# Kernel optimization log

Hardware: AMD Instinct MI355X
Metric: run time of the kernel (lower is better)

The kernel has to match this reference:

```python
import jax, jax.numpy as jnp
import numpy as np

EPS = 1e-5  # BatchNorm1d default eps

def _conv1d(x, w, stride, pad):
    # x: [B, Cin, L], w: [Cout, Cin, K]
    return jax.lax.conv_general_dilated(
        x, w, window_strides=(stride,), padding=[(pad, pad)],
        dimension_numbers=('NCH', 'OIH', 'NCH'))

def _bn(x, g, b, m, v):
    # eval-mode BatchNorm1d with running stats; x: [B, C, L]
    scale = g / jnp.sqrt(v + EPS)
    return x * scale[None, :, None] + (b - m * scale)[None, :, None]

def _hardtanh(x):
    return jnp.clip(x, -1.0, 1.0)

def _maxpool2(x):
    B, C, L = x.shape
    return x.reshape(B, C, L // 2, 2).max(axis=-1)


def setup_inputs() -> dict:
    key = jax.random.key(0)
    ks = jax.random.split(key, 20)
    B, L = 256, 16384
    x = jax.random.normal(ks[0], (B, 1, L), dtype=jnp.float32)
    rms = jax.random.uniform(ks[1], (B, 1), dtype=jnp.float32)
    # conv weights (fan-in scaled)
    w1 = jax.random.normal(ks[2], (16, 1, 17), dtype=jnp.float32) * (1.0 / np.sqrt(1 * 17))
    w2 = jax.random.normal(ks[3], (32, 16, 9), dtype=jnp.float32) * (1.0 / np.sqrt(16 * 9))
    w3 = jax.random.normal(ks[4], (64, 32, 5), dtype=jnp.float32) * (1.0 / np.sqrt(32 * 5))
    # batchnorm params (eval mode: gamma, beta, running mean/var)
    def bn_params(k, C):
        k1, k2, k3, k4 = jax.random.split(k, 4)
        g = 1.0 + 0.1 * jax.random.normal(k1, (C,), dtype=jnp.float32)
        b = 0.1 * jax.random.normal(k2, (C,), dtype=jnp.float32)
        m = 0.1 * jax.random.normal(k3, (C,), dtype=jnp.float32)
        v = jax.random.uniform(k4, (C,), dtype=jnp.float32, minval=0.5, maxval=1.5)
        return g, b, m, v
    g1, b1, m1, v1 = bn_params(ks[5], 16)
    g2, b2, m2, v2 = bn_params(ks[6], 32)
    g3, b3, m3, v3 = bn_params(ks[7], 64)
    fc1_w = jax.random.normal(ks[8], (32, 65), dtype=jnp.float32) * (1.0 / np.sqrt(65))
    fc1_b = jnp.zeros((32,), dtype=jnp.float32)
    fc2_w = jax.random.normal(ks[9], (2, 32), dtype=jnp.float32) * (1.0 / np.sqrt(32))
    fc2_b = jnp.zeros((2,), dtype=jnp.float32)
    return dict(x=x, rms=rms, w1=w1, g1=g1, b1=b1, m1=m1, v1=v1,
                w2=w2, g2=g2, b2=b2, m2=m2, v2=v2,
                w3=w3, g3=g3, b3=b3, m3=m3, v3=v3,
                fc1_w=fc1_w, fc1_b=fc1_b, fc2_w=fc2_w, fc2_b=fc2_b)


def reference(x, rms, w1, g1, b1, m1, v1, w2, g2, b2, m2, v2,
              w3, g3, b3, m3, v3, fc1_w, fc1_b, fc2_w, fc2_b):
    # Stage 1: float conv
    h = _conv1d(x, w1, 2, 8)                 # [B,16,8192]
    h = _maxpool2(_hardtanh(_bn(h, g1, b1, m1, v1)))  # [B,16,4096]
    # Stage 2: binarized (sign) weight conv
    h = _conv1d(h, jnp.sign(w2), 2, 4)       # [B,32,2048]
    h = _maxpool2(_hardtanh(_bn(h, g2, b2, m2, v2)))  # [B,32,1024]
    # Stage 3: binarized weight conv
    h = _conv1d(h, jnp.sign(w3), 2, 2)       # [B,64,512]
    h = _maxpool2(_hardtanh(_bn(h, g3, b3, m3, v3)))  # [B,64,256]
    feat = h.mean(axis=-1)                   # AdaptiveAvgPool1d(1) -> [B,64]
    combined = jnp.concatenate([feat, rms], axis=1)   # [B,65]
    h = _hardtanh(combined @ fc1_w.T + fc1_b)
    return h @ fc2_w.T + fc2_b               # [B,2]
```

## Files before the change

### kernel.cpp

```cpp
#include <hip/hip_runtime.h>
#include <hip/hip_bf16.h>

#define EPS 1e-5f

typedef float f32x4 __attribute__((ext_vector_type(4)));
typedef short s16x8 __attribute__((ext_vector_type(8)));

union FragU { uint4 u; s16x8 s; };

__device__ __forceinline__ float ht(float x){ return __builtin_amdgcn_fmed3f(x, -1.f, 1.f); }
__device__ __forceinline__ float sgn(float v){ return (v>0.f)?1.f:((v<0.f)?-1.f:0.f); }
__device__ __forceinline__ unsigned short f2bf(float f){
    unsigned int u = __builtin_bit_cast(unsigned int, f);
    u += 0x7FFFu + ((u>>16)&1u);
    return (unsigned short)(u>>16);
}
__device__ __forceinline__ unsigned pkbf(float a, float b){
    __hip_bfloat162 h = __float22bfloat162_rn(float2{a, b});
    unsigned u;
    __builtin_memcpy(&u, &h, sizeof(u));
    return u;
}

__global__ __launch_bounds__(512) void prep(
    const float* __restrict__ w1, const float* __restrict__ w2, const float* __restrict__ w3,
    const float* g1,const float* b1,const float* m1,const float* v1,
    const float* g2,const float* b2,const float* m2,const float* v2,
    const float* g3,const float* b3,const float* m3,const float* v3,
    unsigned short* __restrict__ a1, unsigned short* __restrict__ a2,
    unsigned short* __restrict__ a3, float* __restrict__ bn){
  const int t = threadIdx.x, bid = blockIdx.x;
  if(bid == 0){
    if(t < 64){
      int q = t>>4, m = t&15;
      #pragma unroll
      for(int j=0;j<8;++j){ int k = 8*q+j;
        a1[t*8+j] = f2bf((k<17)? w1[m*17+k] : 0.f); }
    }
    if(t<16){ float s = g1[t]*rsqrtf(v1[t]+EPS); bn[t]    = s; bn[16+t]  = b1[t]-m1[t]*s; }
    if(t<32){ float s = g2[t]*rsqrtf(v2[t]+EPS); bn[32+t] = s; bn[64+t]  = b2[t]-m2[t]*s; }
    if(t<64){ float s = g3[t]*rsqrtf(v3[t]+EPS); bn[96+t] = s; bn[160+t] = b3[t]-m3[t]*s; }
  } else if(bid <= 2){
    int e = (bid-1)*512 + t;
    if(e < 640){
      int m = e&15, q = (e>>4)&3, hc = e>>6, c = hc%5, h = hc/5;
      int oc = m + 16*h, k = 2*c + (q>>1);
      #pragma unroll
      for(int j=0;j<8;++j){ int ic = 8*(q&1)+j;
        a2[e*8+j] = f2bf((k<9)? sgn(w2[(oc*16+ic)*9+k]) : 0.f); }
    }
  } else {
    int e = (bid-3)*512 + t;
    if(e < 1280){
      int m = e&15, q = (e>>4)&3, gc = e>>6, c = gc%5, g = gc/5;
      int oc = m + 16*g;
      #pragma unroll
      for(int j=0;j<8;++j){ int ic = 8*q+j;
        a3[e*8+j] = f2bf(sgn(w3[(oc*32+ic)*5+c])); }
    }
  }
}

__global__ __launch_bounds__(256, 4) void kfused(const float* __restrict__ x,
    const unsigned short* __restrict__ a1, const unsigned short* __restrict__ a2,
    const unsigned short* __restrict__ a3, const float* __restrict__ bn,
    float* __restrict__ partial){
  __shared__ __align__(16) unsigned short xs[1216];
  __shared__ __align__(16) unsigned short s1[296*26];
  __shared__ __align__(16) unsigned short s2[68*42];
  __shared__ float fws[4*32];
  const int b  = blockIdx.x >> 3;
  const int tp = blockIdx.x & 7;
  const int tid = threadIdx.x;
  const int m = tid & 15, q = (tid & 63) >> 4, w = tid >> 6;
  const int tw = w & 1, gw = w >> 1;
  const float* xrow = &x[b*16384];

  FragU af1; af1.u = *(const uint4*)&a1[(q*16+m)*8];
  const float sc1 = bn[m], sh1 = bn[16+m];

  for(int u = 0; u < 2; ++u){
    const int t  = 2*tp + u;
    const int Q0 = 16*t;

    const int x0 = 64*Q0 - 56;
    for(int i = tid; i < 304; i += 256){
      int g0 = x0 + 4*i;
      float4 v = make_float4(0.f,0.f,0.f,0.f);
      if(g0 >= 0 && g0 <= 16380) v = *(const float4*)&xrow[g0];
      uint2 pk;
      pk.x = pkbf(v.x, v.y);
      pk.y = pkbf(v.z, v.w);
      *(uint2*)&xs[4*i] = pk;
    }
    __syncthreads();

    const unsigned* X32 = (const unsigned*)xs;
    #pragma unroll 2
    for(int it = 0; it < 10; ++it){
      int tile = it*4 + w;
      if(tile < 37){
        int d = tile*16 + m + 4*q;
        FragU bf;
        bf.u.x = X32[d]; bf.u.y = X32[d+1]; bf.u.z = X32[d+2]; bf.u.w = X32[d+3];
        f32x4 acc = {0.f,0.f,0.f,0.f};
        acc = __builtin_amdgcn_mfma_f32_16x16x32_bf16(bf.s, af1.s, acc, 0,0,0);
        float v0 = ht(acc[0]*sc1 + sh1);
        float v1 = ht(acc[1]*sc1 + sh1);
        float v2 = ht(acc[2]*sc1 + sh1);
        float v3 = ht(acc[3]*sc1 + sh1);
        int ppl = tile*8 + 2*q;
        int gp  = 16*Q0 - 12 + ppl;
        float p0 = ((unsigned)gp     < 4096u) ? fmaxf(v0, v1) : 0.f;
        float p1 = ((unsigned)(gp+1) < 4096u) ? fmaxf(v2, v3) : 0.f;
        unsigned uu = pkbf(p0, p1);
        s1[ppl*26 + m]     = (unsigned short)uu;
        s1[(ppl+1)*26 + m] = (unsigned short)(uu >> 16);
      }
    }
    __syncthreads();

    FragU af2[2][5];
    #pragma unroll
    for(int h=0;h<2;++h)
      #pragma unroll
      for(int c=0;c<5;++c)
        af2[h][c].u = *(const uint4*)&a2[(((h*5+c)*4+q)*16+m)*8];
    float sc2[2], sh2[2];
    #pragma unroll
    for(int h=0;h<2;++h){
      sc2[h] = bn[32 + m + 16*h];
      sh2[h] = bn[64 + m + 16*h];
    }
    #pragma unroll
    for(int it = 0; it < 3; ++it){
      int tile = it*4 + w;
      if(tile < 9){
        int nl = tile*16 + m;
        f32x4 acc[2] = {{0.f,0.f,0.f,0.f},{0.f,0.f,0.f,0.f}};
        #pragma unroll
        for(int c=0;c<5;++c){
          int row = 2*nl + 2*c + (q>>1);
          FragU bf; bf.u = *(const uint4*)&s1[row*26 + 8*(q&1)];
          acc[0] = __builtin_amdgcn_mfma_f32_16x16x32_bf16(bf.s, af2[0][c].s, acc[0],0,0,0);
          acc[1] = __builtin_amdgcn_mfma_f32_16x16x32_bf16(bf.s, af2[1][c].s, acc[1],0,0,0);
        }
        int ppl = tile*8 + 2*q;
        int gp  = 4*Q0 - 2 + ppl;
        bool ok0 = (unsigned)gp     < 1024u;
        bool ok1 = (unsigned)(gp+1) < 1024u;
        #pragma unroll
        for(int h=0;h<2;++h){
          float v0 = ht(acc[h][0]*sc2[h] + sh2[h]);
          float v1 = ht(acc[h][1]*sc2[h] + sh2[h]);
          float v2 = ht(acc[h][2]*sc2[h] + sh2[h]);
          float v3 = ht(acc[h][3]*sc2[h] + sh2[h]);
          float p0 = ok0 ? fmaxf(v0, v1) : 0.f;
          float p1 = ok1 ? fmaxf(v2, v3) : 0.f;
          unsigned uu = pkbf(p0, p1);
          if(ppl < 68){
            s2[ppl*42 + m + 16*h]     = (unsigned short)uu;
            s2[(ppl+1)*42 + m + 16*h] = (unsigned short)(uu >> 16);
          }
        }
      }
    }
    __syncthreads();

    FragU af3[2][5];
    #pragma unroll
    for(int gl=0;gl<2;++gl)
      #pragma unroll
      for(int c=0;c<5;++c)
        af3[gl][c].u = *(const uint4*)&a3[((((2*gw+gl)*5+c)*4+q)*16+m)*8];
    float sc3[2], sh3[2];
    #pragma unroll
    for(int gl=0;gl<2;++gl){
      sc3[gl] = bn[96  + m + 16*(2*gw+gl)];
      sh3[gl] = bn[160 + m + 16*(2*gw+gl)];
    }
    {
      int nl = tw*16 + m;
      f32x4 acc[2] = {{0.f,0.f,0.f,0.f},{0.f,0.f,0.f,0.f}};
      #pragma unroll
      for(int c=0;c<5;++c){
        int row = 2*nl + c;
        FragU bf; bf.u = *(const uint4*)&s2[row*42 + 8*q];
        acc[0] = __builtin_amdgcn_mfma_f32_16x16x32_bf16(bf.s, af3[0][c].s, acc[0],0,0,0);
        acc[1] = __builtin_amdgcn_mfma_f32_16x16x32_bf16(bf.s, af3[1][c].s, acc[1],0,0,0);
      }
      #pragma unroll
      for(int gl=0;gl<2;++gl){
        float v0 = ht(acc[gl][0]*sc3[gl] + sh3[gl]);
        float v1 = ht(acc[gl][1]*sc3[gl] + sh3[gl]);
        float v2 = ht(acc[gl][2]*sc3[gl] + sh3[gl]);
        float v3 = ht(acc[gl][3]*sc3[gl] + sh3[gl]);
        float sm = fmaxf(v0, v1) + fmaxf(v2, v3);
        sm += __shfl_xor(sm, 16);
        sm += __shfl_xor(sm, 32);
        if(q == 0) fws[w*32 + 16*gl + m] = sm;
      }
    }
    __syncthreads();
    if(tid < 64){
      int ocl = tid & 31, g = tid >> 5;
      float sum = fws[(2*g)*32 + ocl] + fws[(2*g+1)*32 + ocl];
      partial[(b*16 + t)*64 + tid] = sum;
    }
  }
}

__global__ __launch_bounds__(256) void kfc(const float* __restrict__ partial,
    const float* __restrict__ rms, const float* __restrict__ fc1w,
    const float* __restrict__ fc1b, const float* __restrict__ fc2w,
    const float* __restrict__ fc2b, float* __restrict__ out){
  __shared__ float feat[4][64];
  __shared__ float hbuf[4][32];
  const int tid = threadIdx.x;
  const int gr = tid >> 6, lt = tid & 63;
  const int b = blockIdx.x*4 + gr;
  float s = 0.f;
  #pragma unroll
  for(int t = 0; t < 16; ++t) s += partial[(b*16 + t)*64 + lt];
  feat[gr][lt] = s * (1.f/256.f);
  __syncthreads();
  if(lt < 32){
    float acc = fc1b[lt];
    const float* wv = &fc1w[lt*65];
    #pragma unroll
    for(int c = 0; c < 64; ++c) acc += wv[c]*feat[gr][c];
    acc += wv[64]*rms[b];
    hbuf[gr][lt] = ht(acc);
  }
  __syncthreads();
  if(lt < 2){
    float acc = fc2b[lt];
    const float* wv = &fc2w[lt*32];
    #pragma unroll
    for(int j = 0; j < 32; ++j) acc += wv[j]*hbuf[gr][j];
    out[b*2 + lt] = acc;
  }
}

extern "C" void kernel_launch(void* const* d_in, const int* in_sizes, int n_in,
                              void* d_out, int out_size, void* d_ws, size_t ws_size,
                              hipStream_t stream){
  (void)in_sizes; (void)n_in; (void)out_size; (void)ws_size;
  const float* x    = (const float*)d_in[0];
  const float* rms  = (const float*)d_in[1];
  const float* w1   = (const float*)d_in[2];
  const float* g1   = (const float*)d_in[3];
  const float* b1   = (const float*)d_in[4];
  const float* m1   = (const float*)d_in[5];
  const float* v1   = (const float*)d_in[6];
  const float* w2   = (const float*)d_in[7];
  const float* g2   = (const float*)d_in[8];
  const float* b2   = (const float*)d_in[9];
  const float* m2   = (const float*)d_in[10];
  const float* v2   = (const float*)d_in[11];
  const float* w3   = (const float*)d_in[12];
  const float* g3   = (const float*)d_in[13];
  const float* b3   = (const float*)d_in[14];
  const float* m3   = (const float*)d_in[15];
  const float* v3   = (const float*)d_in[16];
  const float* fc1w = (const float*)d_in[17];
  const float* fc1b = (const float*)d_in[18];
  const float* fc2w = (const float*)d_in[19];
  const float* fc2b = (const float*)d_in[20];
  float* out  = (float*)d_out;

  float*          partial = (float*)d_ws;
  unsigned short* a1  = (unsigned short*)(partial + 262144);
  unsigned short* a2  = a1 + 512;
  unsigned short* a3  = a2 + 5120;
  float*          bnp = (float*)(a3 + 10240);

  prep<<<6,    512, 0, stream>>>(w1, w2, w3, g1,b1,m1,v1, g2,b2,m2,v2, g3,b3,m3,v3,
                                 a1, a2, a3, bnp);
  kfused<<<2048, 256, 0, stream>>>(x, a1, a2, a3, bnp, partial);
  kfc<<<64, 256, 0, stream>>>(partial, rms, fc1w, fc1b, fc2w, fc2b, out);
}
```

Before: 128.0 us.

## Load conv1 input directly from global into MFMA fragments and double grid

Removes the shared-memory staging buffer for the input signal. Each lane now loads its float2 pairs straight from global memory and packs them into bf16 MFMA fragments, which drops one barrier and the LDS round trip. The per-block two-tile loop is also unrolled into one tile per block, so the grid doubles to 4096 blocks and each block does less serial work. The cost is redundant overlapping global reads across lanes (mostly served by cache) and per-tile bounds checks at the sequence edges.

```diff
diff --git a/kernel.cpp b/kernel.cpp
--- a/kernel.cpp
+++ b/kernel.cpp
@@ -65,148 +65,149 @@
     const unsigned short* __restrict__ a1, const unsigned short* __restrict__ a2,
     const unsigned short* __restrict__ a3, const float* __restrict__ bn,
     float* __restrict__ partial){
-  __shared__ __align__(16) unsigned short xs[1216];
   __shared__ __align__(16) unsigned short s1[296*26];
   __shared__ __align__(16) unsigned short s2[68*42];
   __shared__ float fws[4*32];
-  const int b  = blockIdx.x >> 3;
-  const int tp = blockIdx.x & 7;
+  const int b  = blockIdx.x >> 4;
+  const int t  = blockIdx.x & 15;
+  const int Q0 = 16*t;
   const int tid = threadIdx.x;
   const int m = tid & 15, q = (tid & 63) >> 4, w = tid >> 6;
-  const int tw = w & 1, gw = w >> 1;
   const float* xrow = &x[b*16384];
 
   FragU af1; af1.u = *(const uint4*)&a1[(q*16+m)*8];
   const float sc1 = bn[m], sh1 = bn[16+m];
 
-  for(int u = 0; u < 2; ++u){
-    const int t  = 2*tp + u;
-    const int Q0 = 16*t;
-
-    const int x0 = 64*Q0 - 56;
-    for(int i = tid; i < 304; i += 256){
-      int g0 = x0 + 4*i;
-      float4 v = make_float4(0.f,0.f,0.f,0.f);
-      if(g0 >= 0 && g0 <= 16380) v = *(const float4*)&xrow[g0];
-      uint2 pk;
-      pk.x = pkbf(v.x, v.y);
-      pk.y = pkbf(v.z, v.w);
-      *(uint2*)&xs[4*i] = pk;
-    }
-    __syncthreads();
-
-    const unsigned* X32 = (const unsigned*)xs;
-    #pragma unroll 2
-    for(int it = 0; it < 10; ++it){
-      int tile = it*4 + w;
-      if(tile < 37){
-        int d = tile*16 + m + 4*q;
-        FragU bf;
-        bf.u.x = X32[d]; bf.u.y = X32[d+1]; bf.u.z = X32[d+2]; bf.u.w = X32[d+3];
-        f32x4 acc = {0.f,0.f,0.f,0.f};
-        acc = __builtin_amdgcn_mfma_f32_16x16x32_bf16(bf.s, af1.s, acc, 0,0,0);
-        float v0 = ht(acc[0]*sc1 + sh1);
-        float v1 = ht(acc[1]*sc1 + sh1);
-        float v2 = ht(acc[2]*sc1 + sh1);
-        float v3 = ht(acc[3]*sc1 + sh1);
-        int ppl = tile*8 + 2*q;
-        int gp  = 16*Q0 - 12 + ppl;
-        float p0 = ((unsigned)gp     < 4096u) ? fmaxf(v0, v1) : 0.f;
-        float p1 = ((unsigned)(gp+1) < 4096u) ? fmaxf(v2, v3) : 0.f;
-        unsigned uu = pkbf(p0, p1);
-        s1[ppl*26 + m]     = (unsigned short)uu;
-        s1[(ppl+1)*26 + m] = (unsigned short)(uu >> 16);
+  const int x0 = 64*Q0 - 56;
+  const bool safe = (x0 >= 0) && (x0 <= 15170);
+  const int gbase = x0 + 2*m + 8*q;
+  #pragma unroll 2
+  for(int it = 0; it < 10; ++it){
+    int tile = it*4 + w;
+    if(tile < 37){
+      int g = gbase + 32*tile;
+      float2 f0, f1, f2, f3;
+      if(safe){
+        f0 = *(const float2*)&xrow[g];
+        f1 = *(const float2*)&xrow[g+2];
+        f2 = *(const float2*)&xrow[g+4];
+        f3 = *(const float2*)&xrow[g+6];
+      } else {
+        f0 = f1 = f2 = f3 = make_float2(0.f, 0.f);
+        if((unsigned)g     <= 16382u) f0 = *(const float2*)&xrow[g];
+        if((unsigned)(g+2) <= 16382u) f1 = *(const float2*)&xrow[g+2];
+        if((unsigned)(g+4) <= 16382u) f2 = *(const float2*)&xrow[g+4];
+        if((unsigned)(g+6) <= 16382u) f3 = *(const float2*)&xrow[g+6];
       }
-    }
-    __syncthreads();
-
-    FragU af2[2][5];
-    #pragma unroll
-    for(int h=0;h<2;++h)
-      #pragma unroll
-      for(int c=0;c<5;++c)
-        af2[h][c].u = *(const uint4*)&a2[(((h*5+c)*4+q)*16+m)*8];
-    float sc2[2], sh2[2];
-    #pragma unroll
-    for(int h=0;h<2;++h){
-      sc2[h] = bn[32 + m + 16*h];
-      sh2[h] = bn[64 + m + 16*h];
-    }
-    #pragma unroll
-    for(int it = 0; it < 3; ++it){
-      int tile = it*4 + w;
-      if(tile < 9){
-        int nl = tile*16 + m;
-        f32x4 acc[2] = {{0.f,0.f,0.f,0.f},{0.f,0.f,0.f,0.f}};
-        #pragma unroll
-        for(int c=0;c<5;++c){
-          int row = 2*nl + 2*c + (q>>1);
-          FragU bf; bf.u = *(const uint4*)&s1[row*26 + 8*(q&1)];
-          acc[0] = __builtin_amdgcn_mfma_f32_16x16x32_bf16(bf.s, af2[0][c].s, acc[0],0,0,0);
-          acc[1] = __builtin_amdgcn_mfma_f32_16x16x32_bf16(bf.s, af2[1][c].s, acc[1],0,0,0);
-        }
-        int ppl = tile*8 + 2*q;
-        int gp  = 4*Q0 - 2 + ppl;
-        bool ok0 = (unsigned)gp     < 1024u;
-        bool ok1 = (unsigned)(gp+1) < 1024u;
-        #pragma unroll
-        for(int h=0;h<2;++h){
-          float v0 = ht(acc[h][0]*sc2[h] + sh2[h]);
-          float v1 = ht(acc[h][1]*sc2[h] + sh2[h]);
-          float v2 = ht(acc[h][2]*sc2[h] + sh2[h]);
-          float v3 = ht(acc[h][3]*sc2[h] + sh2[h]);
-          float p0 = ok0 ? fmaxf(v0, v1) : 0.f;
-          float p1 = ok1 ? fmaxf(v2, v3) : 0.f;
-          unsigned uu = pkbf(p0, p1);
-          if(ppl < 68){
-            s2[ppl*42 + m + 16*h]     = (unsigned short)uu;
-            s2[(ppl+1)*42 + m + 16*h] = (unsigned short)(uu >> 16);
-          }
+      FragU bf;
+      bf.u.x = pkbf(f0.x, f0.y);
+      bf.u.y = pkbf(f1.x, f1.y);
+      bf.u.z = pkbf(f2.x, f2.y);
+      bf.u.w = pkbf(f3.x, f3.y);
+      f32x4 acc = {0.f,0.f,0.f,0.f};
+      acc = __builtin_amdgcn_mfma_f32_16x16x32_bf16(bf.s, af1.s, acc, 0,0,0);
+      float v0 = ht(acc[0]*sc1 + sh1);
+      float v1 = ht(acc[1]*sc1 + sh1);
+      float v2 = ht(acc[2]*sc1 + sh1);
+      float v3 = ht(acc[3]*sc1 + sh1);
+      int ppl = tile*8 + 2*q;
+      int gp  = 16*Q0 - 12 + ppl;
+      float p0 = ((unsigned)gp     < 4096u) ? fmaxf(v0, v1) : 0.f;
+      float p1 = ((unsigned)(gp+1) < 4096u) ? fmaxf(v2, v3) : 0.f;
+      unsigned u = pkbf(p0, p1);
+      s1[ppl*26 + m]     = (unsigned short)u;
+      s1[(ppl+1)*26 + m] = (unsigned short)(u >> 16);
+    }
+  }
+  __syncthreads();
+
+  FragU af2[2][5];
+  #pragma unroll
+  for(int h=0;h<2;++h)
+    #pragma unroll
+    for(int c=0;c<5;++c)
+      af2[h][c].u = *(const uint4*)&a2[(((h*5+c)*4+q)*16+m)*8];
+  float sc2[2], sh2[2];
+  #pragma unroll
+  for(int h=0;h<2;++h){
+    sc2[h] = bn[32 + m + 16*h];
+    sh2[h] = bn[64 + m + 16*h];
+  }
+  #pragma unroll
+  for(int it = 0; it < 3; ++it){
+    int tile = it*4 + w;
+    if(tile < 9){
+      int nl = tile*16 + m;
+      f32x4 acc[2] = {{0.f,0.f,0.f,0.f},{0.f,0.f,0.f,0.f}};
+      #pragma unroll
+      for(int c=0;c<5;++c){
+        int row = 2*nl + 2*c + (q>>1);
+        FragU bf; bf.u = *(const uint4*)&s1[row*26 + 8*(q&1)];
+        acc[0] = __builtin_amdgcn_mfma_f32_16x16x32_bf16(bf.s, af2[0][c].s, acc[0],0,0,0);
+        acc[1] = __builtin_amdgcn_mfma_f32_16x16x32_bf16(bf.s, af2[1][c].s, acc[1],0,0,0);
+      }
+      int ppl = tile*8 + 2*q;
+      int gp  = 4*Q0 - 2 + ppl;
+      bool ok0 = (unsigned)gp     < 1024u;
+      bool ok1 = (unsigned)(gp+1) < 1024u;
+      #pragma unroll
+      for(int h=0;h<2;++h){
+        float v0 = ht(acc[h][0]*sc2[h] + sh2[h]);
+        float v1 = ht(acc[h][1]*sc2[h] + sh2[h]);
+        float v2 = ht(acc[h][2]*sc2[h] + sh2[h]);
+        float v3 = ht(acc[h][3]*sc2[h] + sh2[h]);
+        float p0 = ok0 ? fmaxf(v0, v1) : 0.f;
+        float p1 = ok1 ? fmaxf(v2, v3) : 0.f;
+        unsigned u = pkbf(p0, p1);
+        if(ppl < 68){
+          s2[ppl*42 + m + 16*h]     = (unsigned short)u;
+          s2[(ppl+1)*42 + m + 16*h] = (unsigned short)(u >> 16);
         }
       }
     }
-    __syncthreads();
-
-    FragU af3[2][5];
-    #pragma unroll
-    for(int gl=0;gl<2;++gl)
-      #pragma unroll
-      for(int c=0;c<5;++c)
-        af3[gl][c].u = *(const uint4*)&a3[((((2*gw+gl)*5+c)*4+q)*16+m)*8];
-    float sc3[2], sh3[2];
+  }
+  __syncthreads();
+
+  const int tw = w & 1, gw = w >> 1;
+  FragU af3[2][5];
+  #pragma unroll
+  for(int gl=0;gl<2;++gl)
+    #pragma unroll
+    for(int c=0;c<5;++c)
+      af3[gl][c].u = *(const uint4*)&a3[((((2*gw+gl)*5+c)*4+q)*16+m)*8];
+  float sc3[2], sh3[2];
+  #pragma unroll
+  for(int gl=0;gl<2;++gl){
+    sc3[gl] = bn[96  + m + 16*(2*gw+gl)];
+    sh3[gl] = bn[160 + m + 16*(2*gw+gl)];
+  }
+  {
+    int nl = tw*16 + m;
+    f32x4 acc[2] = {{0.f,0.f,0.f,0.f},{0.f,0.f,0.f,0.f}};
+    #pragma unroll
+    for(int c=0;c<5;++c){
+      int row = 2*nl + c;
+      FragU bf; bf.u = *(const uint4*)&s2[row*42 + 8*q];
+      acc[0] = __builtin_amdgcn_mfma_f32_16x16x32_bf16(bf.s, af3[0][c].s, acc[0],0,0,0);
+      acc[1] = __builtin_amdgcn_mfma_f32_16x16x32_bf16(bf.s, af3[1][c].s, acc[1],0,0,0);
+    }
     #pragma unroll
     for(int gl=0;gl<2;++gl){
-      sc3[gl] = bn[96  + m + 16*(2*gw+gl)];
-      sh3[gl] = bn[160 + m + 16*(2*gw+gl)];
-    }
-    {
-      int nl = tw*16 + m;
-      f32x4 acc[2] = {{0.f,0.f,0.f,0.f},{0.f,0.f,0.f,0.f}};
-      #pragma unroll
-      for(int c=0;c<5;++c){
-        int row = 2*nl + c;
-        FragU bf; bf.u = *(const uint4*)&s2[row*42 + 8*q];
-        acc[0] = __builtin_amdgcn_mfma_f32_16x16x32_bf16(bf.s, af3[0][c].s, acc[0],0,0,0);
-        acc[1] = __builtin_amdgcn_mfma_f32_16x16x32_bf16(bf.s, af3[1][c].s, acc[1],0,0,0);
-      }
-      #pragma unroll
-      for(int gl=0;gl<2;++gl){
-        float v0 = ht(acc[gl][0]*sc3[gl] + sh3[gl]);
-        float v1 = ht(acc[gl][1]*sc3[gl] + sh3[gl]);
-        float v2 = ht(acc[gl][2]*sc3[gl] + sh3[gl]);
-        float v3 = ht(acc[gl][3]*sc3[gl] + sh3[gl]);
-        float sm = fmaxf(v0, v1) + fmaxf(v2, v3);
-        sm += __shfl_xor(sm, 16);
-        sm += __shfl_xor(sm, 32);
-        if(q == 0) fws[w*32 + 16*gl + m] = sm;
-      }
-    }
-    __syncthreads();
-    if(tid < 64){
-      int ocl = tid & 31, g = tid >> 5;
-      float sum = fws[(2*g)*32 + ocl] + fws[(2*g+1)*32 + ocl];
-      partial[(b*16 + t)*64 + tid] = sum;
-    }
+      float v0 = ht(acc[gl][0]*sc3[gl] + sh3[gl]);
+      float v1 = ht(acc[gl][1]*sc3[gl] + sh3[gl]);
+      float v2 = ht(acc[gl][2]*sc3[gl] + sh3[gl]);
+      float v3 = ht(acc[gl][3]*sc3[gl] + sh3[gl]);
+      float sm = fmaxf(v0, v1) + fmaxf(v2, v3);
+      sm += __shfl_xor(sm, 16);
+      sm += __shfl_xor(sm, 32);
+      if(q == 0) fws[w*32 + 16*gl + m] = sm;
+    }
+  }
+  __syncthreads();
+  if(tid < 64){
+    int ocl = tid & 31, g = tid >> 5;
+    float sum = fws[(2*g)*32 + ocl] + fws[(2*g+1)*32 + ocl];
+    partial[(b*16 + t)*64 + tid] = sum;
   }
 }
 
@@ -277,6 +278,6 @@
 
   prep<<<6,    512, 0, stream>>>(w1, w2, w3, g1,b1,m1,v1, g2,b2,m2,v2, g3,b3,m3,v3,
                                  a1, a2, a3, bnp);
-  kfused<<<2048, 256, 0, stream>>>(x, a1, a2, a3, bnp, partial);
+  kfused<<<4096, 256, 0, stream>>>(x, a1, a2, a3, bnp, partial);
   kfc<<<64, 256, 0, stream>>>(partial, rms, fc1w, fc1b, fc2w, fc2b, out);
 }
```

After: 137.9 us. 7.8% more time.
